# Optimization experiments

Measured on AMD Instinct MI355X. Metric: run time of the kernel, lower is better.

## Reference

```python
import jax, jax.numpy as jnp
import numpy as np

EPS = 1e-7  # K.epsilon()
ROUTINGS = 3


def squash(v, axis=-1):
    s2 = jnp.sum(jnp.square(v), axis=axis, keepdims=True)
    scale = s2 / (1.0 + s2) / jnp.sqrt(s2 + EPS)
    return scale * v


def setup_inputs() -> dict:
    key = jax.random.key(0)
    k1, k2 = jax.random.split(key)
    B, Ni, Di, No, Do = 64, 2048, 16, 32, 16
    inputs = jax.random.normal(k1, (B, Ni, Di), dtype=jnp.float32)
    # glorot-uniform-ish scale for W
    limit = np.sqrt(6.0 / (Di + Do)).astype(np.float32)
    W = jax.random.uniform(k2, (1, Ni, No, Do, Di), dtype=jnp.float32,
                           minval=-limit, maxval=limit)
    return {"inputs": inputs, "W": W}


def reference(inputs, W):
    # inputs: [B, Ni, Di]; W: [1, Ni, No, Do, Di]
    # inputs_hat[b,n,o,d] = sum_i W[n,o,d,i] * inputs[b,n,i]  -> [B, Ni, No, Do]
    inputs_hat = jnp.einsum('bni,nodi->bnod', inputs, W[0])
    B, Ni, No, _ = inputs_hat.shape
    b = jnp.zeros((B, Ni, No), dtype=inputs_hat.dtype)
    outputs = None
    for i in range(ROUTINGS):
        c = jax.nn.softmax(b, axis=2)              # [B, Ni, No]
        s = jnp.einsum('bnod,bno->bod', inputs_hat, c)  # weighted sum over Ni
        outputs = squash(s)                        # [B, No, Do]
        if i < ROUTINGS - 1:
            # NOTE: faithful to source — update uses sum over Do of c-weighted
            # inputs_hat (does NOT use `outputs`).
            b = b + jnp.sum(inputs_hat * c[..., None], axis=-1)
    return outputs
```

## Files before the change

kernel.cpp:

```cpp
#include <hip/hip_runtime.h>
#include <cmath>


#define NI 2048
#define NGROUPS 256
#define NPER 8

typedef short bf16x8 __attribute__((ext_vector_type(8)));
typedef float f32x4 __attribute__((ext_vector_type(4)));

static __device__ __forceinline__ unsigned cvt_pk_bf16(float a, float b) {
  unsigned r;
  asm("v_cvt_pk_bf16_f32 %0, %1, %2" : "=v"(r) : "v"(a), "v"(b));
  return r;
}
static __device__ __forceinline__ void split4_pk(float4 v, uint2& hi, uint2& lo) {
  hi.x = cvt_pk_bf16(v.x, v.y);
  hi.y = cvt_pk_bf16(v.z, v.w);
  float r0 = v.x - __uint_as_float(hi.x << 16);
  float r1 = v.y - __uint_as_float(hi.x & 0xFFFF0000u);
  float r2 = v.z - __uint_as_float(hi.y << 16);
  float r3 = v.w - __uint_as_float(hi.y & 0xFFFF0000u);
  lo.x = cvt_pk_bf16(r0, r1);
  lo.y = cvt_pk_bf16(r2, r3);
}
static __device__ __forceinline__ int swz8(int r, int u) {
  return r * 8 + ((u ^ ((r >> 2) & 1)) << 2);
}
static __device__ __forceinline__ void barrier_lds() {
  asm volatile("s_waitcnt lgkmcnt(0)" ::: "memory");
  __builtin_amdgcn_s_barrier();
  __builtin_amdgcn_sched_barrier(0);
}

#define WAOFF 0
#define XLOFF 8192
#define HOFF  12288
#define C2OFF 13344
#define LDSZ  14400
__global__ __launch_bounds__(512, 4) void caps_fused_kernel(
    const float* __restrict__ x, const float* __restrict__ W,
    float* __restrict__ partial)
{
  const int bx = blockIdx.x;
  const int xcd = bx & 7, slot = bx >> 3;
  const int ng = xcd * 32 + (slot >> 1);
  const int bh = slot & 1;
  const int t = threadIdx.x;
  const int wv = t >> 6, l = t & 63;
  const int q = l >> 4, dq = l & 15, qh = q & 1, s_a = q >> 1;
  const int bt = wv & 1, oq = wv >> 1;

  __shared__ __align__(16) float lds[LDSZ];
  float* WA  = lds + WAOFF;
  float* XL  = lds + XLOFF;
  float* hS  = lds + HOFF;
  float* c2S = lds + C2OFF;

  float sacc[8][4];
  #pragma unroll
  for (int oo = 0; oo < 8; ++oo)
    { sacc[oo][0] = 0.f; sacc[oo][1] = 0.f; sacc[oo][2] = 0.f; sacc[oo][3] = 0.f; }

  const int n0 = ng * NPER;
  const int wd = (t >> 2) & 15, wi4 = t & 3;
  const int wu = wi4 >> 1, wsub = (wi4 & 1) * 2;

  float4 wreg[4];
  #pragma unroll
  for (int c = 0; c < 4; ++c)
    wreg[c] = *(const float4*)(W + (size_t)n0 * 8192 + c * 2048 + 4 * t);

  #pragma unroll
  for (int m = 0; m < 2; ++m) {
    const int idx = m * 512 + t;
    const int pb = idx >> 5, pn = (idx >> 2) & 7, pi4 = idx & 3;
    float4 v = *(const float4*)(x + (size_t)(bh * 32 + pb) * (NI * 16)
                                 + (n0 + pn) * 16 + pi4 * 4);
    uint2 hi, lo;
    split4_pk(v, hi, lo);
    const int pu = pi4 >> 1, psub = (pi4 & 1) * 2;
    float* XLn = XL + pn * 512;
    *(uint2*)&XLn[swz8(pb, pu) + psub] = hi;
    *(uint2*)&XLn[swz8(32 + pb, pu) + psub] = lo;
  }

  #pragma unroll
  for (int c = 0; c < 4; ++c) {
    uint2 hi, lo;
    split4_pk(wreg[c], hi, lo);
    const int rh = (c * 8 + wv) * 32 + wd;
    *(uint2*)&WA[swz8(rh, wu) + wsub] = hi;
    *(uint2*)&WA[swz8(rh + 16, wu) + wsub] = lo;
  }
  barrier_lds();

  {
    const size_t nb = (size_t)(n0 + 1);
    #pragma unroll
    for (int c = 0; c < 4; ++c)
      wreg[c] = *(const float4*)(W + nb * 8192 + c * 2048 + 4 * t);
  }

  #pragma unroll 1
  for (int nn = 0; nn < NPER; ++nn) {
    f32x4 Dv[8];
    {
      const float* XLn = XL + nn * 512;
      bf16x8 B0 = *(const bf16x8*)&XLn[swz8(bt * 16 + dq, qh)];
      bf16x8 B1 = *(const bf16x8*)&XLn[swz8(32 + bt * 16 + dq, qh)];
      #pragma unroll
      for (int oo = 0; oo < 8; ++oo) {
        const int o = oq * 8 + oo;
        bf16x8 A = *(const bf16x8*)&WA[swz8(o * 32 + s_a * 16 + dq, qh)];
        f32x4 D = {0.f, 0.f, 0.f, 0.f};
        D = __builtin_amdgcn_mfma_f32_16x16x32_bf16(A, B0, D, 0, 0, 0);
        D = __builtin_amdgcn_mfma_f32_16x16x32_bf16(A, B1, D, 0, 0, 0);
        Dv[oo] = D;
        float hs = D[0] + D[1] + D[2] + D[3];
        hs += __shfl_xor(hs, 16);
        hs += __shfl_xor(hs, 32);
        if (q == 0) hS[(bt * 16 + dq) * 33 + o] = hs;
      }
    }
    barrier_lds();

    if (nn < NPER - 1) {
      #pragma unroll
      for (int c = 0; c < 4; ++c) {
        uint2 hi, lo;
        split4_pk(wreg[c], hi, lo);
        const int rh = (c * 8 + wv) * 32 + wd;
        *(uint2*)&WA[swz8(rh, wu) + wsub] = hi;
        *(uint2*)&WA[swz8(rh + 16, wu) + wsub] = lo;
      }
    }

    {
      const int bl = t >> 4, op = t & 15;
      const float h0 = hS[bl * 33 + op];
      const float h1 = hS[bl * 33 + op + 16];
      const float b10 = h0 * 0.03125f, b11 = h1 * 0.03125f;
      float mx = fmaxf(b10, b11);
      mx = fmaxf(mx, __shfl_xor(mx, 1)); mx = fmaxf(mx, __shfl_xor(mx, 2));
      mx = fmaxf(mx, __shfl_xor(mx, 4)); mx = fmaxf(mx, __shfl_xor(mx, 8));
      const float e0 = __expf(b10 - mx), e1 = __expf(b11 - mx);
      float S = e0 + e1;
      S += __shfl_xor(S, 1); S += __shfl_xor(S, 2);
      S += __shfl_xor(S, 4); S += __shfl_xor(S, 8);
      const float inv = 1.0f / S;
      const float b20 = b10 + e0 * inv * h0, b21 = b11 + e1 * inv * h1;
      float mx2 = fmaxf(b20, b21);
      mx2 = fmaxf(mx2, __shfl_xor(mx2, 1)); mx2 = fmaxf(mx2, __shfl_xor(mx2, 2));
      mx2 = fmaxf(mx2, __shfl_xor(mx2, 4)); mx2 = fmaxf(mx2, __shfl_xor(mx2, 8));
      const float e20 = __expf(b20 - mx2), e21 = __expf(b21 - mx2);
      float S2 = e20 + e21;
      S2 += __shfl_xor(S2, 1); S2 += __shfl_xor(S2, 2);
      S2 += __shfl_xor(S2, 4); S2 += __shfl_xor(S2, 8);
      const float inv2 = 1.0f / S2;
      c2S[op * 33 + bl] = e20 * inv2;
      c2S[(op + 16) * 33 + bl] = e21 * inv2;
    }

    if (nn < NPER - 2) {
      const size_t nb = (size_t)(n0 + nn + 2);
      #pragma unroll
      for (int c = 0; c < 4; ++c)
        wreg[c] = *(const float4*)(W + nb * 8192 + c * 2048 + 4 * t);
    }
    barrier_lds();

    #pragma unroll
    for (int oo = 0; oo < 8; ++oo) {
      const int o = oq * 8 + oo;
      const float c = c2S[o * 33 + bt * 16 + dq];
      sacc[oo][0] += c * Dv[oo][0]; sacc[oo][1] += c * Dv[oo][1];
      sacc[oo][2] += c * Dv[oo][2]; sacc[oo][3] += c * Dv[oo][3];
    }
  }

  float* pb = partial + (size_t)ng * 32768
            + (size_t)(bh * 32 + bt * 16 + dq) * 512 + q * 4;
  #pragma unroll
  for (int oo = 0; oo < 8; ++oo) {
    const int o = oq * 8 + oo;
    *(float4*)(pb + o * 16)
        = make_float4(sacc[oo][0], sacc[oo][1], sacc[oo][2], sacc[oo][3]);
  }
}

__global__ __launch_bounds__(256) void caps_reduce_kernel(
    const float* __restrict__ partial, float* __restrict__ out)
{
  const int t = threadIdx.x;
  const int w4 = t >> 6, ln = t & 63;
  const int pair = blockIdx.x * 4 + w4;
  const int b = pair >> 5, o = pair & 31;
  const int d = ln & 15, cg = ln >> 4;
  const float* p = partial + (size_t)b * 512 + o * 16 + d;
  float s = 0.f;
  #pragma unroll 8
  for (int gg = cg; gg < NGROUPS; gg += 4) s += p[(size_t)gg * 32768];
  s += __shfl_xor(s, 16); s += __shfl_xor(s, 32);
  float s2 = s * s;
  s2 += __shfl_xor(s2, 1); s2 += __shfl_xor(s2, 2);
  s2 += __shfl_xor(s2, 4); s2 += __shfl_xor(s2, 8);
  float scale = s2 / (1.0f + s2) / sqrtf(s2 + 1e-7f);
  if (ln < 16) out[(size_t)b * 512 + o * 16 + d] = scale * s;
}

extern "C" void kernel_launch(void* const* d_in, const int* in_sizes, int n_in,
                              void* d_out, int out_size, void* d_ws, size_t ws_size,
                              hipStream_t stream) {
  const float* x = (const float*)d_in[0];
  const float* W = (const float*)d_in[1];
  if (in_sizes[0] != 64 * 2048 * 16) { const float* tmp = x; x = W; W = tmp; }
  float* out = (float*)d_out;

  float* partial = (float*)d_ws;

  caps_fused_kernel<<<512, 512, 0, stream>>>(x, W, partial);
  caps_reduce_kernel<<<512, 256, 0, stream>>>(partial, out);
}
```

Measured before the change: 127.0 us.

## Load W fragments directly into registers, drop LDS staging, use DPP reductions

Each lane now loads its own W rows straight from global memory into registers and builds the bf16 hi/lo MFMA A-fragments in place, with a two-deep software prefetch across o and n. This removes the LDS staging buffer for W, its split-and-store pass, and one dependency on the barrier, and it shrinks shared memory. Softmax reductions across 16 lanes switch from shuffles to DPP row rotations. The cost is redundant global loads and bf16 conversions, since each W element is now fetched by both bt wave halves and converted for both hi and lo in every lane. Register pressure also rises.

```diff
diff --git a/kernel.cpp b/kernel.cpp
--- a/kernel.cpp
+++ b/kernel.cpp
@@ -32,12 +32,43 @@
   __builtin_amdgcn_s_barrier();
   __builtin_amdgcn_sched_barrier(0);
 }
-
-#define WAOFF 0
-#define XLOFF 8192
-#define HOFF  12288
-#define C2OFF 13344
-#define LDSZ  14400
+template<int CTRL>
+static __device__ __forceinline__ float dpp_rot(float v) {
+  return __int_as_float(__builtin_amdgcn_mov_dpp(__float_as_int(v), CTRL, 0xF, 0xF, true));
+}
+static __device__ __forceinline__ float sum16_dpp(float v) {
+  v += dpp_rot<0x128>(v); v += dpp_rot<0x124>(v);
+  v += dpp_rot<0x122>(v); v += dpp_rot<0x121>(v);
+  return v;
+}
+static __device__ __forceinline__ float max16_dpp(float v) {
+  v = fmaxf(v, dpp_rot<0x128>(v)); v = fmaxf(v, dpp_rot<0x124>(v));
+  v = fmaxf(v, dpp_rot<0x122>(v)); v = fmaxf(v, dpp_rot<0x121>(v));
+  return v;
+}
+static __device__ __forceinline__ bf16x8 mk_afrag(float4 v0, float4 v1, bool lo) {
+  unsigned h0 = cvt_pk_bf16(v0.x, v0.y), h1 = cvt_pk_bf16(v0.z, v0.w);
+  unsigned h2 = cvt_pk_bf16(v1.x, v1.y), h3 = cvt_pk_bf16(v1.z, v1.w);
+  float r0 = v0.x - __uint_as_float(h0 << 16);
+  float r1 = v0.y - __uint_as_float(h0 & 0xFFFF0000u);
+  float r2 = v0.z - __uint_as_float(h1 << 16);
+  float r3 = v0.w - __uint_as_float(h1 & 0xFFFF0000u);
+  float r4 = v1.x - __uint_as_float(h2 << 16);
+  float r5 = v1.y - __uint_as_float(h2 & 0xFFFF0000u);
+  float r6 = v1.z - __uint_as_float(h3 << 16);
+  float r7 = v1.w - __uint_as_float(h3 & 0xFFFF0000u);
+  unsigned g0 = cvt_pk_bf16(r0, r1), g1 = cvt_pk_bf16(r2, r3);
+  unsigned g2 = cvt_pk_bf16(r4, r5), g3 = cvt_pk_bf16(r6, r7);
+  union { unsigned u[4]; bf16x8 v; } a;
+  a.u[0] = lo ? g0 : h0; a.u[1] = lo ? g1 : h1;
+  a.u[2] = lo ? g2 : h2; a.u[3] = lo ? g3 : h3;
+  return a.v;
+}
+
+#define XLOFF 0
+#define HOFF  4096
+#define C2OFF 5152
+#define LDSZ  6208
 __global__ __launch_bounds__(512, 4) void caps_fused_kernel(
     const float* __restrict__ x, const float* __restrict__ W,
     float* __restrict__ partial)
@@ -48,11 +79,11 @@
   const int bh = slot & 1;
   const int t = threadIdx.x;
   const int wv = t >> 6, l = t & 63;
-  const int q = l >> 4, dq = l & 15, qh = q & 1, s_a = q >> 1;
+  const int q = l >> 4, dq = l & 15, qh = q & 1;
+  const bool s_lo = (q >> 1) != 0;
   const int bt = wv & 1, oq = wv >> 1;
 
   __shared__ __align__(16) float lds[LDSZ];
-  float* WA  = lds + WAOFF;
   float* XL  = lds + XLOFF;
   float* hS  = lds + HOFF;
   float* c2S = lds + C2OFF;
@@ -63,13 +94,7 @@
     { sacc[oo][0] = 0.f; sacc[oo][1] = 0.f; sacc[oo][2] = 0.f; sacc[oo][3] = 0.f; }
 
   const int n0 = ng * NPER;
-  const int wd = (t >> 2) & 15, wi4 = t & 3;
-  const int wu = wi4 >> 1, wsub = (wi4 & 1) * 2;
-
-  float4 wreg[4];
-  #pragma unroll
-  for (int c = 0; c < 4; ++c)
-    wreg[c] = *(const float4*)(W + (size_t)n0 * 8192 + c * 2048 + 4 * t);
+  const float* wlane = W + (size_t)dq * 16 + qh * 8 + (size_t)(oq * 8) * 256;
 
   #pragma unroll
   for (int m = 0; m < 2; ++m) {
@@ -84,23 +109,13 @@
     *(uint2*)&XLn[swz8(pb, pu) + psub] = hi;
     *(uint2*)&XLn[swz8(32 + pb, pu) + psub] = lo;
   }
-
-  #pragma unroll
-  for (int c = 0; c < 4; ++c) {
-    uint2 hi, lo;
-    split4_pk(wreg[c], hi, lo);
-    const int rh = (c * 8 + wv) * 32 + wd;
-    *(uint2*)&WA[swz8(rh, wu) + wsub] = hi;
-    *(uint2*)&WA[swz8(rh + 16, wu) + wsub] = lo;
+  float4 wv0[2], wv1[2];
+  {
+    const float* p0 = wlane + (size_t)n0 * 8192;
+    wv0[0] = *(const float4*)(p0);           wv1[0] = *(const float4*)(p0 + 4);
+    wv0[1] = *(const float4*)(p0 + 256);     wv1[1] = *(const float4*)(p0 + 260);
   }
   barrier_lds();
-
-  {
-    const size_t nb = (size_t)(n0 + 1);
-    #pragma unroll
-    for (int c = 0; c < 4; ++c)
-      wreg[c] = *(const float4*)(W + nb * 8192 + c * 2048 + 4 * t);
-  }
 
   #pragma unroll 1
   for (int nn = 0; nn < NPER; ++nn) {
@@ -111,8 +126,14 @@
       bf16x8 B1 = *(const bf16x8*)&XLn[swz8(32 + bt * 16 + dq, qh)];
       #pragma unroll
       for (int oo = 0; oo < 8; ++oo) {
-        const int o = oq * 8 + oo;
-        bf16x8 A = *(const bf16x8*)&WA[swz8(o * 32 + s_a * 16 + dq, qh)];
+        bf16x8 A = mk_afrag(wv0[oo & 1], wv1[oo & 1], s_lo);
+        if (oo < 6) {
+          const float* p = wlane + (size_t)(n0 + nn) * 8192 + (oo + 2) * 256;
+          wv0[oo & 1] = *(const float4*)p;  wv1[oo & 1] = *(const float4*)(p + 4);
+        } else if (nn < NPER - 1) {
+          const float* p = wlane + (size_t)(n0 + nn + 1) * 8192 + (oo - 6) * 256;
+          wv0[oo & 1] = *(const float4*)p;  wv1[oo & 1] = *(const float4*)(p + 4);
+        }
         f32x4 D = {0.f, 0.f, 0.f, 0.f};
         D = __builtin_amdgcn_mfma_f32_16x16x32_bf16(A, B0, D, 0, 0, 0);
         D = __builtin_amdgcn_mfma_f32_16x16x32_bf16(A, B1, D, 0, 0, 0);
@@ -120,60 +141,33 @@
         float hs = D[0] + D[1] + D[2] + D[3];
         hs += __shfl_xor(hs, 16);
         hs += __shfl_xor(hs, 32);
-        if (q == 0) hS[(bt * 16 + dq) * 33 + o] = hs;
+        if (q == 0) hS[(bt * 16 + dq) * 33 + (oq * 8 + oo)] = hs;
       }
     }
     barrier_lds();
-
-    if (nn < NPER - 1) {
-      #pragma unroll
-      for (int c = 0; c < 4; ++c) {
-        uint2 hi, lo;
-        split4_pk(wreg[c], hi, lo);
-        const int rh = (c * 8 + wv) * 32 + wd;
-        *(uint2*)&WA[swz8(rh, wu) + wsub] = hi;
-        *(uint2*)&WA[swz8(rh + 16, wu) + wsub] = lo;
-      }
-    }
 
     {
       const int bl = t >> 4, op = t & 15;
       const float h0 = hS[bl * 33 + op];
       const float h1 = hS[bl * 33 + op + 16];
       const float b10 = h0 * 0.03125f, b11 = h1 * 0.03125f;
-      float mx = fmaxf(b10, b11);
-      mx = fmaxf(mx, __shfl_xor(mx, 1)); mx = fmaxf(mx, __shfl_xor(mx, 2));
-      mx = fmaxf(mx, __shfl_xor(mx, 4)); mx = fmaxf(mx, __shfl_xor(mx, 8));
+      const float mx = max16_dpp(fmaxf(b10, b11));
       const float e0 = __expf(b10 - mx), e1 = __expf(b11 - mx);
-      float S = e0 + e1;
-      S += __shfl_xor(S, 1); S += __shfl_xor(S, 2);
-      S += __shfl_xor(S, 4); S += __shfl_xor(S, 8);
+      const float S = sum16_dpp(e0 + e1);
       const float inv = 1.0f / S;
       const float b20 = b10 + e0 * inv * h0, b21 = b11 + e1 * inv * h1;
-      float mx2 = fmaxf(b20, b21);
-      mx2 = fmaxf(mx2, __shfl_xor(mx2, 1)); mx2 = fmaxf(mx2, __shfl_xor(mx2, 2));
-      mx2 = fmaxf(mx2, __shfl_xor(mx2, 4)); mx2 = fmaxf(mx2, __shfl_xor(mx2, 8));
+      const float mx2 = max16_dpp(fmaxf(b20, b21));
       const float e20 = __expf(b20 - mx2), e21 = __expf(b21 - mx2);
-      float S2 = e20 + e21;
-      S2 += __shfl_xor(S2, 1); S2 += __shfl_xor(S2, 2);
-      S2 += __shfl_xor(S2, 4); S2 += __shfl_xor(S2, 8);
+      const float S2 = sum16_dpp(e20 + e21);
       const float inv2 = 1.0f / S2;
       c2S[op * 33 + bl] = e20 * inv2;
       c2S[(op + 16) * 33 + bl] = e21 * inv2;
     }
-
-    if (nn < NPER - 2) {
-      const size_t nb = (size_t)(n0 + nn + 2);
-      #pragma unroll
-      for (int c = 0; c < 4; ++c)
-        wreg[c] = *(const float4*)(W + nb * 8192 + c * 2048 + 4 * t);
-    }
     barrier_lds();
 
     #pragma unroll
     for (int oo = 0; oo < 8; ++oo) {
-      const int o = oq * 8 + oo;
-      const float c = c2S[o * 33 + bt * 16 + dq];
+      const float c = c2S[(oq * 8 + oo) * 33 + bt * 16 + dq];
       sacc[oo][0] += c * Dv[oo][0]; sacc[oo][1] += c * Dv[oo][1];
       sacc[oo][2] += c * Dv[oo][2]; sacc[oo][3] += c * Dv[oo][3];
     }
@@ -183,8 +177,7 @@
             + (size_t)(bh * 32 + bt * 16 + dq) * 512 + q * 4;
   #pragma unroll
   for (int oo = 0; oo < 8; ++oo) {
-    const int o = oq * 8 + oo;
-    *(float4*)(pb + o * 16)
+    *(float4*)(pb + (oq * 8 + oo) * 16)
         = make_float4(sacc[oo][0], sacc[oo][1], sacc[oo][2], sacc[oo][3]);
   }
 }
```

New measurement: 140.2 us. 1.1x slower.
